# Optimization experiments

Measured on AMD Instinct MI355X. Metric: run time of the kernel, lower is better.

## Reference

```python
import jax, jax.numpy as jnp
import numpy as np

EPS = 1e-5  # torch BatchNorm1d default eps
CATAGORY = 2


def setup_inputs() -> dict:
    key = jax.random.key(0)
    ks = jax.random.split(key, 8)
    B, N, D, P = 64, 512, 512, 720
    return {
        "x": jax.random.normal(ks[0], (B, N, D), dtype=jnp.float32),
        "W_exp": jax.random.normal(ks[1], (CATAGORY, D, P), dtype=jnp.float32) * 0.02,
        "b_exp": jax.random.normal(ks[2], (CATAGORY, P), dtype=jnp.float32) * 0.02,
        "W1": jax.random.normal(ks[3], (D, 128), dtype=jnp.float32) * 0.05,
        "b1": jnp.zeros((128,), jnp.float32),
        "g1": jnp.ones((128,), jnp.float32),
        "be1": jnp.zeros((128,), jnp.float32),
        "m1": jnp.zeros((128,), jnp.float32),
        "v1": jnp.ones((128,), jnp.float32),
        "W2": jax.random.normal(ks[4], (128, 32), dtype=jnp.float32) * 0.1,
        "b2": jnp.zeros((32,), jnp.float32),
        "g2": jnp.ones((32,), jnp.float32),
        "be2": jnp.zeros((32,), jnp.float32),
        "m2": jnp.zeros((32,), jnp.float32),
        "v2": jnp.ones((32,), jnp.float32),
        "W3": jax.random.normal(ks[5], (32, 1), dtype=jnp.float32) * 0.1,
        "b3": jnp.zeros((1,), jnp.float32),
    }


def _bn(h, gamma, beta, mean, var):
    # BatchNorm1d, eval mode (running stats); dropout is identity in eval
    return (h - mean) * jax.lax.rsqrt(var + EPS) * gamma + beta


def reference(x, W_exp, b_exp, W1, b1, g1, be1, m1, v1,
              W2, b2, g2, be2, m2, v2, W3, b3):
    B, N, D = x.shape
    xf = x.reshape(B * N, D)
    # classifier: Linear -> BN -> ReLU -> Linear -> BN -> ReLU -> Linear -> Sigmoid
    h = jax.nn.relu(_bn(xf @ W1 + b1, g1, be1, m1, v1))
    h = jax.nn.relu(_bn(h @ W2 + b2, g2, be2, m2, v2))
    z = jax.nn.sigmoid(h @ W3 + b3).reshape(B, N)  # [B, N] class score
    # per-token expert index (sigmoid score rounded to {0, 1})
    idx = jnp.clip(jnp.round(z), 0, CATAGORY - 1).astype(jnp.int32)  # [B, N]
    # compute all experts (catagory=2, cheap) then gather per-token choice
    outs = jnp.einsum("bnd,edp->bnep", x, W_exp) + b_exp  # [B, N, E, P]
    sel = jnp.take_along_axis(outs, idx[:, :, None, None], axis=2)
    return sel[:, :, 0, :]  # [B, N, pred_len]
```

## Files before the change

kernel.cpp:

```cpp
#include <hip/hip_runtime.h>

#define DEV __device__ __forceinline__

typedef __bf16 bf16x8 __attribute__((ext_vector_type(8)));
typedef float f32x4 __attribute__((ext_vector_type(4)));
typedef float f32x2 __attribute__((ext_vector_type(2)));

constexpr int TOK = 32768;
constexpr int D   = 512;
constexpr int P   = 720;
constexpr float EPS = 1e-5f;

DEV unsigned short f2bf(float f) {
  unsigned u = __float_as_uint(f);
  u += 0x7FFFu + ((u >> 16) & 1u);
  return (unsigned short)(u >> 16);
}

DEV void g2lds16(const void* g, void* l) {
  __builtin_amdgcn_global_load_lds(
      (__attribute__((address_space(1))) void*)g,
      (__attribute__((address_space(3))) void*)l, 16, 0, 0);
}

__global__ void wconv_kernel(const float* __restrict__ W,
                             unsigned short* __restrict__ WT) {
  __shared__ float ls[16][17];
  const int e  = blockIdx.z;
  const int d0 = blockIdx.x * 16, p0 = blockIdx.y * 16;
  const int tx = threadIdx.x, ty = threadIdx.y;
  ls[ty][tx] = W[((size_t)e * D + d0 + ty) * P + p0 + tx];
  __syncthreads();
  WT[((size_t)e * P + p0 + ty) * D + d0 + tx] = f2bf(ls[tx][ty]);
}

__global__ __launch_bounds__(256, 3) void classifier_kernel(
    const float* __restrict__ x,
    const float* __restrict__ W1, const float* __restrict__ b1,
    const float* __restrict__ g1, const float* __restrict__ be1,
    const float* __restrict__ m1, const float* __restrict__ v1,
    const float* __restrict__ W2, const float* __restrict__ b2,
    const float* __restrict__ g2, const float* __restrict__ be2,
    const float* __restrict__ m2, const float* __restrict__ v2,
    const float* __restrict__ W3, const float* __restrict__ b3,
    unsigned short* __restrict__ xb, int* __restrict__ idx_out)
{
  constexpr int TM = 64, BK = 32;
  __shared__ __align__(16) char smem[50176];
  float (*xs)[32][68]  = (float(*)[32][68])smem;
  float (*ws)[32][128] = (float(*)[32][128])(smem + 17408);
  float (*h1s)[68]     = (float(*)[68])smem;
  float (*h2s)[68]     = (float(*)[68])(smem + 34816);

  const int tid  = threadIdx.x;
  const int wave = tid >> 6;
  const int lane = tid & 63;
  const int t0   = blockIdx.x * TM;

  const int xr = tid >> 2;
  const int xc = (tid & 3) * 4;
  const int tg = tid >> 4;
  const int cc = tid & 15;

  f32x2 acc[2][8];
  #pragma unroll
  for (int p = 0; p < 2; ++p)
    #pragma unroll
    for (int j = 0; j < 8; ++j) acc[p][j] = (f32x2)0.f;

  float4 px0, px1;

  auto issue_x = [&](int kt) {
    const float* base = &x[(size_t)(t0 + xr) * D + kt * BK + xc];
    px0 = *reinterpret_cast<const float4*>(base);
    px1 = *reinterpret_cast<const float4*>(base + 16);
  };
  auto commit_x = [&](int b, int kt) {
    xs[b][xc + 0][xr] = px0.x;  xs[b][xc + 1][xr] = px0.y;
    xs[b][xc + 2][xr] = px0.z;  xs[b][xc + 3][xr] = px0.w;
    xs[b][xc + 16][xr] = px1.x; xs[b][xc + 17][xr] = px1.y;
    xs[b][xc + 18][xr] = px1.z; xs[b][xc + 19][xr] = px1.w;
    ushort4 u0, u1;
    u0.x = f2bf(px0.x); u0.y = f2bf(px0.y); u0.z = f2bf(px0.z); u0.w = f2bf(px0.w);
    u1.x = f2bf(px1.x); u1.y = f2bf(px1.y); u1.z = f2bf(px1.z); u1.w = f2bf(px1.w);
    unsigned short* xbase = &xb[(size_t)(t0 + xr) * D + kt * BK + xc];
    *reinterpret_cast<ushort4*>(xbase)      = u0;
    *reinterpret_cast<ushort4*>(xbase + 16) = u1;
  };
  auto issue_w = [&](int b, int kt) {
    char* ldsbase = (char*)&ws[b][0][0];
    const int kk = (lane >> 5);
    const int ch = (lane & 31) * 4;
    #pragma unroll
    for (int i = 0; i < 4; ++i) {
      const int op = wave * 4 + i;
      g2lds16(&W1[(size_t)(kt * BK + op * 2 + kk) * 128 + ch],
              (char*)ldsbase + op * 1024);
    }
  };

  issue_w(0, 0);
  issue_x(0);
  commit_x(0, 0);
  __syncthreads();

  int buf = 0;
  for (int kt = 0; kt < D / BK; ++kt) {
    const int nb = buf ^ 1;
    if (kt < D / BK - 1) {
      issue_w(nb, kt + 1);
      issue_x(kt + 1);
    }
    #pragma unroll 4
    for (int kk = 0; kk < BK; ++kk) {
      const f32x4 xv = *reinterpret_cast<const f32x4*>(&xs[buf][kk][tg * 4]);
      const f32x4 wa = *reinterpret_cast<const f32x4*>(&ws[buf][kk][cc * 4]);
      const f32x4 wb = *reinterpret_cast<const f32x4*>(&ws[buf][kk][64 + cc * 4]);
      f32x2 xp[2];
      xp[0][0] = xv[0]; xp[0][1] = xv[1];
      xp[1][0] = xv[2]; xp[1][1] = xv[3];
      const float wr[8] = {wa[0], wa[1], wa[2], wa[3], wb[0], wb[1], wb[2], wb[3]};
      #pragma unroll
      for (int p = 0; p < 2; ++p)
        #pragma unroll
        for (int j = 0; j < 8; ++j) {
          f32x2 wv = {wr[j], wr[j]};
          acc[p][j] = __builtin_elementwise_fma(xp[p], wv, acc[p][j]);
        }
    }
    if (kt < D / BK - 1) commit_x(nb, kt + 1);
    __syncthreads();
    buf = nb;
  }

  #pragma unroll
  for (int j = 0; j < 8; ++j) {
    const int col = (j < 4) ? (cc * 4 + j) : (60 + cc * 4 + j);
    const float A  = g1[col] / sqrtf(v1[col] + EPS);
    const float Bc = (b1[col] - m1[col]) * A + be1[col];
    float4 hv;
    hv.x = fmaxf(0.f, fmaf(acc[0][j][0], A, Bc));
    hv.y = fmaxf(0.f, fmaf(acc[0][j][1], A, Bc));
    hv.z = fmaxf(0.f, fmaf(acc[1][j][0], A, Bc));
    hv.w = fmaxf(0.f, fmaf(acc[1][j][1], A, Bc));
    *reinterpret_cast<float4*>(&h1s[col][tg * 4]) = hv;
  }
  __syncthreads();

  {
    const int c2 = (tid & 7) * 4;
    const int t2 = (tid >> 3) * 2;
    f32x2 a2[4];
    #pragma unroll
    for (int c = 0; c < 4; ++c) a2[c] = (f32x2)0.f;
    #pragma unroll 8
    for (int j = 0; j < 128; ++j) {
      const f32x2 h = *reinterpret_cast<const f32x2*>(&h1s[j][t2]);
      const float4 w = *reinterpret_cast<const float4*>(&W2[j * 32 + c2]);
      const float wr[4] = {w.x, w.y, w.z, w.w};
      #pragma unroll
      for (int c = 0; c < 4; ++c) {
        f32x2 wv = {wr[c], wr[c]};
        a2[c] = __builtin_elementwise_fma(h, wv, a2[c]);
      }
    }
    #pragma unroll
    for (int c = 0; c < 4; ++c) {
      const int col = c2 + c;
      const float A  = g2[col] / sqrtf(v2[col] + EPS);
      const float Bc = (b2[col] - m2[col]) * A + be2[col];
      f32x2 hv;
      hv[0] = fmaxf(0.f, fmaf(a2[c][0], A, Bc));
      hv[1] = fmaxf(0.f, fmaf(a2[c][1], A, Bc));
      *reinterpret_cast<f32x2*>(&h2s[col][t2]) = hv;
    }
  }
  __syncthreads();

  if (tid < TM) {
    float logit = b3[0];
    #pragma unroll
    for (int k = 0; k < 32; ++k)
      logit = fmaf(h2s[k][tid], W3[k], logit);
    idx_out[t0 + tid] = (logit > 0.f) ? 1 : 0;
  }
}

__global__ __launch_bounds__(256) void expert_gemm_kernel(
    const unsigned short* __restrict__ xb,
    const unsigned short* __restrict__ WT,
    const float* __restrict__ b_exp,
    const int* __restrict__ idx,
    float* __restrict__ out)
{
  constexpr int GM = 128, GN = 80, GK = 32;
  constexpr int NT = D / GK;
  __shared__ __align__(16) unsigned short As[4][GM * GK];
  __shared__ __align__(16) unsigned short Bs[4][2 * GN * GK];

  const int tid  = threadIdx.x;
  const int wave = tid >> 6;
  const int lane = tid & 63;

  const int wg    = blockIdx.x;
  const int xcd   = wg & 7;
  const int local = wg >> 3;
  const int t0 = (xcd * 32 + local / 9) * GM;
  const int p0 = (local % 9) * GN;

  const int col = lane & 15;
  const int rg  = lane >> 4;

  int er[2][4];
  #pragma unroll
  for (int mf = 0; mf < 2; ++mf)
    #pragma unroll
    for (int j = 0; j < 4; ++j)
      er[mf][j] = idx[t0 + wave * 32 + mf * 16 + rg * 4 + j];
  float be0[5], be1v[5];
  #pragma unroll
  for (int nf = 0; nf < 5; ++nf) {
    be0[nf]  = b_exp[p0 + nf * 16 + col];
    be1v[nf] = b_exp[P + p0 + nf * 16 + col];
  }
  asm volatile("s_waitcnt vmcnt(0)" ::: "memory");

  f32x4 acc[2][2][5];
  #pragma unroll
  for (int e = 0; e < 2; ++e)
    #pragma unroll
    for (int mf = 0; mf < 2; ++mf)
      #pragma unroll
      for (int nf = 0; nf < 5; ++nf) acc[e][mf][nf] = (f32x4)(0.f);

  const int srow = lane >> 2;
  const int sswz = (lane & 3) ^ ((srow >> 1) & 3);

  auto stage = [&](int b, int kt) {
    const int k0 = kt * GK;
    #pragma unroll
    for (int i = 0; i < 5; ++i) {
      const int c = wave + i * 4;
      if (c < 18) {
        if (c < 8) {
          const int row = c * 16 + srow;
          g2lds16(xb + (size_t)(t0 + row) * D + k0 + sswz * 8,
                  (char*)As[b] + c * 1024);
        } else {
          const int cb = c - 8;
          const int e  = (cb >= 5) ? 1 : 0;
          const int bc = cb - e * 5;
          const int pr = bc * 16 + srow;
          g2lds16(WT + ((size_t)e * P + p0 + pr) * D + k0 + sswz * 8,
                  (char*)Bs[b] + e * 5120 + bc * 1024);
        }
      }
    }
  };

  stage(0, 0);
  stage(1, 1);
  stage(2, 2);

  for (int kt = 0; kt < NT; ++kt) {
    if (wave < 2) asm volatile("s_waitcnt vmcnt(10)" ::: "memory");
    else          asm volatile("s_waitcnt vmcnt(8)"  ::: "memory");
    __builtin_amdgcn_s_barrier();
    __builtin_amdgcn_sched_barrier(0);

    if (kt + 3 < NT) stage((kt + 3) & 3, kt + 3);

    const int buf = kt & 3;
    bf16x8 af[2];
    #pragma unroll
    for (int mf = 0; mf < 2; ++mf) {
      const int r  = wave * 32 + mf * 16 + (lane & 15);
      const int ch = (lane >> 4) ^ ((r >> 1) & 3);
      af[mf] = *(const bf16x8*)((const char*)As[buf] + r * 64 + ch * 16);
    }
    #pragma unroll
    for (int e = 0; e < 2; ++e) {
      #pragma unroll
      for (int nf = 0; nf < 5; ++nf) {
        const int pr = nf * 16 + (lane & 15);
        const int ch = (lane >> 4) ^ ((pr >> 1) & 3);
        bf16x8 bfrag = *(const bf16x8*)((const char*)Bs[buf] + e * 5120 + pr * 64 + ch * 16);
        #pragma unroll
        for (int mf = 0; mf < 2; ++mf)
          acc[e][mf][nf] = __builtin_amdgcn_mfma_f32_16x16x32_bf16(
              af[mf], bfrag, acc[e][mf][nf], 0, 0, 0);
      }
    }
  }

  #pragma unroll
  for (int nf = 0; nf < 5; ++nf) {
    const int p = p0 + nf * 16 + col;
    #pragma unroll
    for (int mf = 0; mf < 2; ++mf) {
      #pragma unroll
      for (int j = 0; j < 4; ++j) {
        const int row = wave * 32 + mf * 16 + rg * 4 + j;
        const float v = er[mf][j] ? (acc[1][mf][nf][j] + be1v[nf])
                                  : (acc[0][mf][nf][j] + be0[nf]);
        out[(size_t)(t0 + row) * P + p] = v;
      }
    }
  }
}

extern "C" void kernel_launch(void* const* d_in, const int* in_sizes, int n_in,
                              void* d_out, int out_size, void* d_ws, size_t ws_size,
                              hipStream_t stream) {
  const float* x     = (const float*)d_in[0];
  const float* W_exp = (const float*)d_in[1];
  const float* b_exp = (const float*)d_in[2];
  const float* W1 = (const float*)d_in[3];
  const float* b1 = (const float*)d_in[4];
  const float* g1 = (const float*)d_in[5];
  const float* be1 = (const float*)d_in[6];
  const float* m1 = (const float*)d_in[7];
  const float* v1 = (const float*)d_in[8];
  const float* W2 = (const float*)d_in[9];
  const float* b2 = (const float*)d_in[10];
  const float* g2 = (const float*)d_in[11];
  const float* be2 = (const float*)d_in[12];
  const float* m2 = (const float*)d_in[13];
  const float* v2 = (const float*)d_in[14];
  const float* W3 = (const float*)d_in[15];
  const float* b3 = (const float*)d_in[16];
  float* out = (float*)d_out;

  unsigned short* xb = (unsigned short*)d_ws;
  unsigned short* WT = (unsigned short*)((char*)d_ws + (size_t)TOK * D * 2);
  int* idx = (int*)((char*)d_ws + (size_t)TOK * D * 2 + (size_t)2 * P * D * 2);

  hipLaunchKernelGGL(wconv_kernel, dim3(D / 16, P / 16, 2), dim3(16, 16),
                     0, stream, W_exp, WT);
  hipLaunchKernelGGL(classifier_kernel, dim3(TOK / 64), dim3(256), 0, stream,
                     x, W1, b1, g1, be1, m1, v1, W2, b2, g2, be2, m2, v2, W3, b3,
                     xb, idx);
  hipLaunchKernelGGL(expert_gemm_kernel, dim3((TOK / 128) * (P / 80)), dim3(256),
                     0, stream, xb, WT, b_exp, idx, out);
}
```

Measured before the change: 141.8 us.

## Route tokens into per-expert lists and compute only the selected expert GEMM

The classifier now appends each token to a per-expert list using atomic counters instead of writing a dense index array. The expert GEMM gathers rows of the bf16 activations by list, multiplies against only the chosen expert's weights, and scatters the results back to each token's output row. Before, both experts were computed for every token and one was discarded, so this removes about half the MFMA work and half the B-tile staging. It adds a memset launch, atomics, gathered A-row loads, scattered stores, a grid sized for the worst case that exits early, and nondeterministic token order within each list.

```diff
diff --git a/kernel.cpp b/kernel.cpp
--- a/kernel.cpp
+++ b/kernel.cpp
@@ -43,7 +43,8 @@
     const float* __restrict__ g2, const float* __restrict__ be2,
     const float* __restrict__ m2, const float* __restrict__ v2,
     const float* __restrict__ W3, const float* __restrict__ b3,
-    unsigned short* __restrict__ xb, int* __restrict__ idx_out)
+    unsigned short* __restrict__ xb, int* __restrict__ cnt,
+    int* __restrict__ lists)
 {
   constexpr int TM = 64, BK = 32;
   __shared__ __align__(16) char smem[50176];
@@ -182,7 +183,9 @@
     #pragma unroll
     for (int k = 0; k < 32; ++k)
       logit = fmaf(h2s[k][tid], W3[k], logit);
-    idx_out[t0 + tid] = (logit > 0.f) ? 1 : 0;
+    const int e = (logit > 0.f) ? 1 : 0;
+    const int pos = atomicAdd(&cnt[e], 1);
+    lists[e * TOK + pos] = t0 + tid;
   }
 }
 
@@ -190,71 +193,86 @@
     const unsigned short* __restrict__ xb,
     const unsigned short* __restrict__ WT,
     const float* __restrict__ b_exp,
-    const int* __restrict__ idx,
+    const int* __restrict__ cnt,
+    const int* __restrict__ lists,
     float* __restrict__ out)
 {
   constexpr int GM = 128, GN = 80, GK = 32;
   constexpr int NT = D / GK;
   __shared__ __align__(16) unsigned short As[4][GM * GK];
-  __shared__ __align__(16) unsigned short Bs[4][2 * GN * GK];
+  __shared__ __align__(16) unsigned short Bs[4][GN * GK];
 
   const int tid  = threadIdx.x;
   const int wave = tid >> 6;
   const int lane = tid & 63;
 
+  const int n0 = cnt[0], n1 = cnt[1];
+  const int T0 = (n0 + GM - 1) >> 7;
+  const int T1 = (n1 + GM - 1) >> 7;
+
   const int wg    = blockIdx.x;
   const int xcd   = wg & 7;
   const int local = wg >> 3;
-  const int t0 = (xcd * 32 + local / 9) * GM;
-  const int p0 = (local % 9) * GN;
-
-  const int col = lane & 15;
-  const int rg  = lane >> 4;
-
-  int er[2][4];
-  #pragma unroll
-  for (int mf = 0; mf < 2; ++mf)
-    #pragma unroll
-    for (int j = 0; j < 4; ++j)
-      er[mf][j] = idx[t0 + wave * 32 + mf * 16 + rg * 4 + j];
-  float be0[5], be1v[5];
-  #pragma unroll
-  for (int nf = 0; nf < 5; ++nf) {
-    be0[nf]  = b_exp[p0 + nf * 16 + col];
-    be1v[nf] = b_exp[P + p0 + nf * 16 + col];
-  }
-  asm volatile("s_waitcnt vmcnt(0)" ::: "memory");
-
-  f32x4 acc[2][2][5];
-  #pragma unroll
-  for (int e = 0; e < 2; ++e)
-    #pragma unroll
-    for (int mf = 0; mf < 2; ++mf)
-      #pragma unroll
-      for (int nf = 0; nf < 5; ++nf) acc[e][mf][nf] = (f32x4)(0.f);
-
+  const int gt    = xcd * 33 + local / 9;
+  const int pt    = local % 9;
+  if (gt >= T0 + T1) return;
+  const int e  = (gt >= T0) ? 1 : 0;
+  const int ne = e ? n1 : n0;
+  const int m0 = (e ? gt - T0 : gt) * GM;
+  const int p0 = pt * GN;
+  const int* lst = lists + e * TOK;
+
+  const int col  = lane & 15;
+  const int rg   = lane >> 4;
   const int srow = lane >> 2;
   const int sswz = (lane & 3) ^ ((srow >> 1) & 3);
 
+  int aid[2];
+  #pragma unroll
+  for (int i = 0; i < 2; ++i) {
+    const int r = (wave + i * 4) * 16 + srow;
+    int g = m0 + r; if (g > ne - 1) g = ne - 1;
+    aid[i] = lst[g];
+  }
+  int eid[2][4]; unsigned evalid = 0;
+  #pragma unroll
+  for (int mf = 0; mf < 2; ++mf)
+    #pragma unroll
+    for (int j = 0; j < 4; ++j) {
+      const int g = m0 + wave * 32 + mf * 16 + rg * 4 + j;
+      const int gc = (g > ne - 1) ? ne - 1 : g;
+      eid[mf][j] = lst[gc];
+      if (g < ne) evalid |= 1u << (mf * 4 + j);
+    }
+  float be[5];
+  #pragma unroll
+  for (int nf = 0; nf < 5; ++nf)
+    be[nf] = b_exp[e * P + p0 + nf * 16 + col];
+  asm volatile("s_waitcnt vmcnt(0)" ::: "memory");
+
+  f32x4 acc[2][5];
+  #pragma unroll
+  for (int mf = 0; mf < 2; ++mf)
+    #pragma unroll
+    for (int nf = 0; nf < 5; ++nf) acc[mf][nf] = (f32x4)(0.f);
+
   auto stage = [&](int b, int kt) {
     const int k0 = kt * GK;
     #pragma unroll
-    for (int i = 0; i < 5; ++i) {
+    for (int i = 0; i < 2; ++i) {
       const int c = wave + i * 4;
-      if (c < 18) {
-        if (c < 8) {
-          const int row = c * 16 + srow;
-          g2lds16(xb + (size_t)(t0 + row) * D + k0 + sswz * 8,
-                  (char*)As[b] + c * 1024);
-        } else {
-          const int cb = c - 8;
-          const int e  = (cb >= 5) ? 1 : 0;
-          const int bc = cb - e * 5;
-          const int pr = bc * 16 + srow;
-          g2lds16(WT + ((size_t)e * P + p0 + pr) * D + k0 + sswz * 8,
-                  (char*)Bs[b] + e * 5120 + bc * 1024);
-        }
-      }
+      g2lds16(xb + (size_t)aid[i] * D + k0 + sswz * 8,
+              (char*)As[b] + c * 1024);
+    }
+    {
+      const int pr = wave * 16 + srow;
+      g2lds16(WT + ((size_t)e * P + p0 + pr) * D + k0 + sswz * 8,
+              (char*)Bs[b] + wave * 1024);
+    }
+    if (wave == 0) {
+      const int pr = 64 + srow;
+      g2lds16(WT + ((size_t)e * P + p0 + pr) * D + k0 + sswz * 8,
+              (char*)Bs[b] + 4 * 1024);
     }
   };
 
@@ -262,9 +280,17 @@
   stage(1, 1);
   stage(2, 2);
 
+  #pragma unroll
   for (int kt = 0; kt < NT; ++kt) {
-    if (wave < 2) asm volatile("s_waitcnt vmcnt(10)" ::: "memory");
-    else          asm volatile("s_waitcnt vmcnt(8)"  ::: "memory");
+    if (kt < NT - 2) {
+      if (wave == 0) asm volatile("s_waitcnt vmcnt(8)" ::: "memory");
+      else           asm volatile("s_waitcnt vmcnt(6)" ::: "memory");
+    } else if (kt == NT - 2) {
+      if (wave == 0) asm volatile("s_waitcnt vmcnt(4)" ::: "memory");
+      else           asm volatile("s_waitcnt vmcnt(3)" ::: "memory");
+    } else {
+      asm volatile("s_waitcnt vmcnt(0)" ::: "memory");
+    }
     __builtin_amdgcn_s_barrier();
     __builtin_amdgcn_sched_barrier(0);
 
@@ -279,17 +305,14 @@
       af[mf] = *(const bf16x8*)((const char*)As[buf] + r * 64 + ch * 16);
     }
     #pragma unroll
-    for (int e = 0; e < 2; ++e) {
+    for (int nf = 0; nf < 5; ++nf) {
+      const int pr = nf * 16 + (lane & 15);
+      const int ch = (lane >> 4) ^ ((pr >> 1) & 3);
+      bf16x8 bfrag = *(const bf16x8*)((const char*)Bs[buf] + pr * 64 + ch * 16);
       #pragma unroll
-      for (int nf = 0; nf < 5; ++nf) {
-        const int pr = nf * 16 + (lane & 15);
-        const int ch = (lane >> 4) ^ ((pr >> 1) & 3);
-        bf16x8 bfrag = *(const bf16x8*)((const char*)Bs[buf] + e * 5120 + pr * 64 + ch * 16);
-        #pragma unroll
-        for (int mf = 0; mf < 2; ++mf)
-          acc[e][mf][nf] = __builtin_amdgcn_mfma_f32_16x16x32_bf16(
-              af[mf], bfrag, acc[e][mf][nf], 0, 0, 0);
-      }
+      for (int mf = 0; mf < 2; ++mf)
+        acc[mf][nf] = __builtin_amdgcn_mfma_f32_16x16x32_bf16(
+            af[mf], bfrag, acc[mf][nf], 0, 0, 0);
     }
   }
 
@@ -300,10 +323,8 @@
     for (int mf = 0; mf < 2; ++mf) {
       #pragma unroll
       for (int j = 0; j < 4; ++j) {
-        const int row = wave * 32 + mf * 16 + rg * 4 + j;
-        const float v = er[mf][j] ? (acc[1][mf][nf][j] + be1v[nf])
-                                  : (acc[0][mf][nf][j] + be0[nf]);
-        out[(size_t)(t0 + row) * P + p] = v;
+        if (evalid & (1u << (mf * 4 + j)))
+          out[(size_t)eid[mf][j] * P + p] = acc[mf][nf][j] + be[nf];
       }
     }
   }
@@ -331,15 +352,18 @@
   const float* b3 = (const float*)d_in[16];
   float* out = (float*)d_out;
 
-  unsigned short* xb = (unsigned short*)d_ws;
-  unsigned short* WT = (unsigned short*)((char*)d_ws + (size_t)TOK * D * 2);
-  int* idx = (int*)((char*)d_ws + (size_t)TOK * D * 2 + (size_t)2 * P * D * 2);
-
+  char* wsb = (char*)d_ws;
+  unsigned short* xb = (unsigned short*)wsb;
+  unsigned short* WT = (unsigned short*)(wsb + 33554432);
+  int* cnt   = (int*)(wsb + 35028992);
+  int* lists = (int*)(wsb + 35029248);
+
+  hipMemsetAsync(cnt, 0, 2 * sizeof(int), stream);
   hipLaunchKernelGGL(wconv_kernel, dim3(D / 16, P / 16, 2), dim3(16, 16),
                      0, stream, W_exp, WT);
   hipLaunchKernelGGL(classifier_kernel, dim3(TOK / 64), dim3(256), 0, stream,
                      x, W1, b1, g1, be1, m1, v1, W2, b2, g2, be2, m2, v2, W3, b3,
-                     xb, idx);
-  hipLaunchKernelGGL(expert_gemm_kernel, dim3((TOK / 128) * (P / 80)), dim3(256),
-                     0, stream, xb, WT, b_exp, idx, out);
-}
+                     xb, cnt, lists);
+  hipLaunchKernelGGL(expert_gemm_kernel, dim3(8 * 33 * 9), dim3(256),
+                     0, stream, xb, WT, b_exp, cnt, lists, out);
+}
```

New measurement: 369.5 us. 2.61x slower.
